# Optimization experiments

Hardware: AMD Instinct MI355X
Metric: run time of the kernel (lower is better)

Reference implementation:

```python
import jax, jax.numpy as jnp
import numpy as np

N_NODES = 50000
N_EDGES = 800000
N_GRAPHS = 256
D_IN, D_H1, D_H2, D_OUT = 64, 64, 64, 64


def gcn_conv(x, W, b, src, dst, n_nodes):
    # PyG GCNConv (eval): h = x @ W; add self-loops; deg[i] = in_deg(i) + 1;
    # out[i] = sum_{j->i} h[j] * deg[i]^-1/2 deg[j]^-1/2 + h[i]/deg[i] + b
    h = x @ W  # [N, F]
    ones = jnp.ones((src.shape[0],), dtype=x.dtype)
    deg = jax.ops.segment_sum(ones, dst, num_segments=n_nodes) + 1.0  # self loop
    dinv = jax.lax.rsqrt(deg)
    norm = dinv[src] * dinv[dst]  # [E]
    msg = h[src] * norm[:, None]  # [E, F]  (memory-bound gather)
    agg = jax.ops.segment_sum(msg, dst, num_segments=n_nodes)  # scatter-add
    agg = agg + h * (1.0 / deg)[:, None]  # self-loop contribution
    return agg + b


def setup_inputs() -> dict:
    key = jax.random.key(0)
    ks = jax.random.split(key, 12)
    x = jax.random.normal(ks[0], (N_NODES, D_IN), dtype=jnp.float32)
    src = jax.random.randint(ks[1], (N_EDGES,), 0, N_NODES)
    dst = jax.random.randint(ks[2], (N_EDGES,), 0, N_NODES)
    batch = jnp.sort(jax.random.randint(ks[3], (N_NODES,), 0, N_GRAPHS))
    def glorot(k, fin, fout):
        s = jnp.sqrt(6.0 / (fin + fout))
        return jax.random.uniform(k, (fin, fout), jnp.float32, -s, s)
    return {
        "x": x, "src": src, "dst": dst, "batch": batch,
        "W1": glorot(ks[4], D_IN, D_H1), "b1": jnp.zeros((D_H1,), jnp.float32),
        "W2": glorot(ks[5], D_H1, D_H2), "b2": jnp.zeros((D_H2,), jnp.float32),
        "W3": glorot(ks[6], D_H2, D_OUT), "b3": jnp.zeros((D_OUT,), jnp.float32),
        "Wl": glorot(ks[7], D_OUT, 1), "bl": jnp.zeros((1,), jnp.float32),
    }


def reference(x, src, dst, batch, W1, b1, W2, b2, W3, b3, Wl, bl):
    n = x.shape[0]
    h = jax.nn.relu(gcn_conv(x, W1, b1, src, dst, n))   # dropout inactive (eval)
    h = jax.nn.relu(gcn_conv(h, W2, b2, src, dst, n))
    h = jax.nn.relu(gcn_conv(h, W3, b3, src, dst, n))
    # global_mean_pool over graph ids
    sums = jax.ops.segment_sum(h, batch, num_segments=N_GRAPHS)  # [G, F]
    cnt = jax.ops.segment_sum(jnp.ones((n,), h.dtype), batch, num_segments=N_GRAPHS)
    pooled = sums / jnp.maximum(cnt, 1.0)[:, None]
    return pooled @ Wl + bl  # [G, 1]
```

## Files before the change

kernel.cpp:

```cpp
#include <hip/hip_runtime.h>

#define N_NODES 50000
#define N_EDGES 800000
#define N_GRAPHS 256
#define F 64
#define NBUCK 196
#define CAP 4608
#define P3_TILE 2048
#define P3_GRID ((N_EDGES + P3_TILE - 1) / P3_TILE)
#define BCAP 6144

__device__ __forceinline__ unsigned short f2bf(float f) {
    union { float f; unsigned u; } c; c.f = f;
    unsigned u = c.u + 0x7FFFu + ((c.u >> 16) & 1u);
    return (unsigned short)(u >> 16);
}
__device__ __forceinline__ unsigned pack2bf(float lo, float hi) {
    return (unsigned)f2bf(lo) | ((unsigned)f2bf(hi) << 16);
}
__device__ __forceinline__ float bfl(unsigned u) {
    union { unsigned u; float f; } c; c.u = u << 16; return c.f;
}
__device__ __forceinline__ float bfh(unsigned u) {
    union { unsigned u; float f; } c; c.u = u & 0xFFFF0000u; return c.f;
}

__global__ __launch_bounds__(256) void partition_edges(const int* __restrict__ src,
                                                       const int* __restrict__ dst,
                                                       int* __restrict__ bcur,
                                                       unsigned int* __restrict__ bpair) {
    __shared__ int bh[NBUCK], bloc[NBUCK], bpos[NBUCK];
    int t = threadIdx.x;
    int lo = blockIdx.x * P3_TILE;
    int hi = min(lo + P3_TILE, N_EDGES);
    for (int i = t; i < NBUCK; i += 256) { bh[i] = 0; bpos[i] = 0; }
    __syncthreads();
    for (int e = lo + t; e < hi; e += 256) atomicAdd(&bh[dst[e] >> 8], 1);
    __syncthreads();
    for (int i = t; i < NBUCK; i += 256)
        bloc[i] = bh[i] ? atomicAdd(&bcur[i], bh[i]) : 0;
    __syncthreads();
    for (int e = lo + t; e < hi; e += 256) {
        int d = dst[e];
        int b = d >> 8;
        int r = atomicAdd(&bpos[b], 1);
        bpair[(size_t)b * CAP + bloc[b] + r] = ((unsigned)src[e] << 8) | (unsigned)(d & 255);
    }
}

__global__ __launch_bounds__(256) void bucket_sort(const unsigned int* __restrict__ bpair,
                                                   const int* __restrict__ bcur,
                                                   int* __restrict__ eidx,
                                                   int* __restrict__ rbeg,
                                                   int* __restrict__ rend,
                                                   float* __restrict__ dinv) {
    __shared__ int cnt[256], s[256], pos[256];
    __shared__ int lout[BCAP];
    int b = blockIdx.x, t = threadIdx.x;
    int base = b * CAP;
    int sz = bcur[b];

    cnt[t] = 0;
    __syncthreads();
    for (int i = t; i < sz; i += 256) atomicAdd(&cnt[bpair[base + i] & 255], 1);
    __syncthreads();
    int v = cnt[t];
    s[t] = v;
    __syncthreads();
    for (int off = 1; off < 256; off <<= 1) {
        int u = (t >= off) ? s[t - off] : 0;
        __syncthreads();
        s[t] += u;
        __syncthreads();
    }
    int excl = s[t] - v;
    pos[t] = excl;
    int node = b * 256 + t;
    if (node < N_NODES) {
        rbeg[node] = base + excl;
        rend[node] = base + excl + v;
        dinv[node] = 1.0f / sqrtf((float)v + 1.0f);
    }
    __syncthreads();

    if (sz <= BCAP) {
        for (int i = t; i < sz; i += 256) {
            unsigned p = bpair[base + i];
            int r = atomicAdd(&pos[p & 255], 1);
            lout[r] = (int)((p >> 8) << 7);
        }
        __syncthreads();
        for (int i = t; i < sz; i += 256) eidx[base + i] = lout[i];
    } else {
        for (int i = t; i < sz; i += 256) {
            unsigned p = bpair[base + i];
            int r = atomicAdd(&pos[p & 255], 1);
            eidx[base + r] = (int)((p >> 8) << 7);
        }
    }
}

#define XSTRIDE 17
template <bool BF16IN>
__global__ __launch_bounds__(256) void gemm64_t(const void* __restrict__ Xv,
                                                const float* __restrict__ W,
                                                const float* __restrict__ dinv,
                                                unsigned short* __restrict__ Hn, int n) {
    __shared__ float4 sW[64 * 16];
    __shared__ float4 sX[128 * XSTRIDE];
    int tid = threadIdx.x;
    int base = blockIdx.x * 128;

    const float4* W4 = (const float4*)W;
    for (int i = tid; i < 64 * 16; i += 256) sW[i] = W4[i];
    if (BF16IN) {
        const uint4* X4 = (const uint4*)Xv;
        for (int i = tid; i < 128 * 8; i += 256) {
            int r = i >> 3, c = i & 7;
            int node = base + r;
            uint4 u = (node < n) ? X4[(size_t)node * 8 + c]
                                 : make_uint4(0u, 0u, 0u, 0u);
            sX[r * XSTRIDE + 2 * c]     = make_float4(bfl(u.x), bfh(u.x), bfl(u.y), bfh(u.y));
            sX[r * XSTRIDE + 2 * c + 1] = make_float4(bfl(u.z), bfh(u.z), bfl(u.w), bfh(u.w));
        }
    } else {
        const float4* X4 = (const float4*)Xv;
        for (int i = tid; i < 128 * 16; i += 256) {
            int r = i >> 4, kg = i & 15;
            int node = base + r;
            sX[r * XSTRIDE + kg] = (node < n) ? X4[(size_t)node * 16 + kg]
                                              : make_float4(0.f, 0.f, 0.f, 0.f);
        }
    }
    __syncthreads();

    int fg = tid & 15;
    int ng = tid >> 4;
    float4 acc[8];
#pragma unroll
    for (int ii = 0; ii < 8; ii++) acc[ii] = make_float4(0.f, 0.f, 0.f, 0.f);

    for (int kg = 0; kg < 16; kg++) {
        float4 xv[8];
#pragma unroll
        for (int ii = 0; ii < 8; ii++) xv[ii] = sX[(ng + 16 * ii) * XSTRIDE + kg];
#pragma unroll
        for (int kk = 0; kk < 4; kk++) {
            float4 wv = sW[(4 * kg + kk) * 16 + fg];
#pragma unroll
            for (int ii = 0; ii < 8; ii++) {
                float xs = (kk == 0) ? xv[ii].x : (kk == 1) ? xv[ii].y
                         : (kk == 2) ? xv[ii].z : xv[ii].w;
                acc[ii].x += wv.x * xs;
                acc[ii].y += wv.y * xs;
                acc[ii].z += wv.z * xs;
                acc[ii].w += wv.w * xs;
            }
        }
    }

    ushort4* H4 = (ushort4*)Hn;
#pragma unroll
    for (int ii = 0; ii < 8; ii++) {
        int node = base + ng + 16 * ii;
        if (node < n) {
            float d = dinv[node];
            float4 o = acc[ii];
            ushort4 u;
            u.x = f2bf(o.x * d); u.y = f2bf(o.y * d);
            u.z = f2bf(o.z * d); u.w = f2bf(o.w * d);
            H4[(size_t)node * 16 + fg] = u;
        }
    }
}

__global__ __launch_bounds__(256) void gather_layer(const int* __restrict__ rbeg,
                                                    const int* __restrict__ rend,
                                                    const int* __restrict__ eidx,
                                                    const float* __restrict__ dinv,
                                                    const unsigned short* __restrict__ Hn,
                                                    const float* __restrict__ b,
                                                    unsigned short* __restrict__ OUT, int n) {
    int wv = (blockIdx.x * blockDim.x + threadIdx.x) >> 6;
    int lane = threadIdx.x & 63;
    int ns = lane >> 3, f = lane & 7;
    int node = wv * 8 + ns;
    bool valid = node < n;
    int beg = valid ? rbeg[node] : 0;
    int end = valid ? rend[node] : 0;
    const char* Hb = (const char*)Hn;

    float a0 = 0.f, a1 = 0.f, a2 = 0.f, a3 = 0.f;
    float a4 = 0.f, a5 = 0.f, a6 = 0.f, a7 = 0.f;
    int k = beg;
    for (; k + 3 < end; k += 4) {
        int o1 = eidx[k], o2 = eidx[k + 1], o3 = eidx[k + 2], o4 = eidx[k + 3];
        uint4 p = *(const uint4*)(Hb + o1 + f * 16);
        uint4 q = *(const uint4*)(Hb + o2 + f * 16);
        uint4 r = *(const uint4*)(Hb + o3 + f * 16);
        uint4 w = *(const uint4*)(Hb + o4 + f * 16);
        a0 += (bfl(p.x) + bfl(q.x)) + (bfl(r.x) + bfl(w.x));
        a1 += (bfh(p.x) + bfh(q.x)) + (bfh(r.x) + bfh(w.x));
        a2 += (bfl(p.y) + bfl(q.y)) + (bfl(r.y) + bfl(w.y));
        a3 += (bfh(p.y) + bfh(q.y)) + (bfh(r.y) + bfh(w.y));
        a4 += (bfl(p.z) + bfl(q.z)) + (bfl(r.z) + bfl(w.z));
        a5 += (bfh(p.z) + bfh(q.z)) + (bfh(r.z) + bfh(w.z));
        a6 += (bfl(p.w) + bfl(q.w)) + (bfl(r.w) + bfl(w.w));
        a7 += (bfh(p.w) + bfh(q.w)) + (bfh(r.w) + bfh(w.w));
    }
    for (; k < end; k++) {
        int o1 = eidx[k];
        uint4 p = *(const uint4*)(Hb + o1 + f * 16);
        a0 += bfl(p.x); a1 += bfh(p.x);
        a2 += bfl(p.y); a3 += bfh(p.y);
        a4 += bfl(p.z); a5 += bfh(p.z);
        a6 += bfl(p.w); a7 += bfh(p.w);
    }

    if (valid) {
        float di = dinv[node];
        uint4 hs = *(const uint4*)(Hb + (size_t)node * 128 + f * 16);
        float4 b0 = ((const float4*)b)[2 * f];
        float4 b1 = ((const float4*)b)[2 * f + 1];
        float v0 = fmaxf(di * (a0 + bfl(hs.x)) + b0.x, 0.f);
        float v1 = fmaxf(di * (a1 + bfh(hs.x)) + b0.y, 0.f);
        float v2 = fmaxf(di * (a2 + bfl(hs.y)) + b0.z, 0.f);
        float v3 = fmaxf(di * (a3 + bfh(hs.y)) + b0.w, 0.f);
        float v4 = fmaxf(di * (a4 + bfl(hs.z)) + b1.x, 0.f);
        float v5 = fmaxf(di * (a5 + bfh(hs.z)) + b1.y, 0.f);
        float v6 = fmaxf(di * (a6 + bfl(hs.w)) + b1.z, 0.f);
        float v7 = fmaxf(di * (a7 + bfh(hs.w)) + b1.w, 0.f);
        uint4 u;
        u.x = pack2bf(v0, v1); u.y = pack2bf(v2, v3);
        u.z = pack2bf(v4, v5); u.w = pack2bf(v6, v7);
        ((uint4*)OUT)[(size_t)node * 8 + f] = u;
    }
}

__global__ __launch_bounds__(256) void gather_pool(const int* __restrict__ rbeg,
                                                   const int* __restrict__ rend,
                                                   const int* __restrict__ eidx,
                                                   const float* __restrict__ dinv,
                                                   const unsigned short* __restrict__ Hn,
                                                   const float* __restrict__ b,
                                                   const float* __restrict__ Wl,
                                                   float* __restrict__ pdot, int n) {
    int wv = (blockIdx.x * blockDim.x + threadIdx.x) >> 6;
    int lane = threadIdx.x & 63;
    int ns = lane >> 3, f = lane & 7;
    int node = wv * 8 + ns;
    bool valid = node < n;
    int beg = valid ? rbeg[node] : 0;
    int end = valid ? rend[node] : 0;
    const char* Hb = (const char*)Hn;

    float a0 = 0.f, a1 = 0.f, a2 = 0.f, a3 = 0.f;
    float a4 = 0.f, a5 = 0.f, a6 = 0.f, a7 = 0.f;
    int k = beg;
    for (; k + 3 < end; k += 4) {
        int o1 = eidx[k], o2 = eidx[k + 1], o3 = eidx[k + 2], o4 = eidx[k + 3];
        uint4 p = *(const uint4*)(Hb + o1 + f * 16);
        uint4 q = *(const uint4*)(Hb + o2 + f * 16);
        uint4 r = *(const uint4*)(Hb + o3 + f * 16);
        uint4 w = *(const uint4*)(Hb + o4 + f * 16);
        a0 += (bfl(p.x) + bfl(q.x)) + (bfl(r.x) + bfl(w.x));
        a1 += (bfh(p.x) + bfh(q.x)) + (bfh(r.x) + bfh(w.x));
        a2 += (bfl(p.y) + bfl(q.y)) + (bfl(r.y) + bfl(w.y));
        a3 += (bfh(p.y) + bfh(q.y)) + (bfh(r.y) + bfh(w.y));
        a4 += (bfl(p.z) + bfl(q.z)) + (bfl(r.z) + bfl(w.z));
        a5 += (bfh(p.z) + bfh(q.z)) + (bfh(r.z) + bfh(w.z));
        a6 += (bfl(p.w) + bfl(q.w)) + (bfl(r.w) + bfl(w.w));
        a7 += (bfh(p.w) + bfh(q.w)) + (bfh(r.w) + bfh(w.w));
    }
    for (; k < end; k++) {
        int o1 = eidx[k];
        uint4 p = *(const uint4*)(Hb + o1 + f * 16);
        a0 += bfl(p.x); a1 += bfh(p.x);
        a2 += bfl(p.y); a3 += bfh(p.y);
        a4 += bfl(p.z); a5 += bfh(p.z);
        a6 += bfl(p.w); a7 += bfh(p.w);
    }

    float di = valid ? dinv[node] : 0.f;
    uint4 hs = valid ? *(const uint4*)(Hb + (size_t)node * 128 + f * 16)
                     : make_uint4(0u, 0u, 0u, 0u);
    float4 b0 = ((const float4*)b)[2 * f];
    float4 b1 = ((const float4*)b)[2 * f + 1];
    float4 w0 = ((const float4*)Wl)[2 * f];
    float4 w1 = ((const float4*)Wl)[2 * f + 1];
    float d = 0.f;
    d += fmaxf(di * (a0 + bfl(hs.x)) + b0.x, 0.f) * w0.x;
    d += fmaxf(di * (a1 + bfh(hs.x)) + b0.y, 0.f) * w0.y;
    d += fmaxf(di * (a2 + bfl(hs.y)) + b0.z, 0.f) * w0.z;
    d += fmaxf(di * (a3 + bfh(hs.y)) + b0.w, 0.f) * w0.w;
    d += fmaxf(di * (a4 + bfl(hs.z)) + b1.x, 0.f) * w1.x;
    d += fmaxf(di * (a5 + bfh(hs.z)) + b1.y, 0.f) * w1.y;
    d += fmaxf(di * (a6 + bfl(hs.w)) + b1.z, 0.f) * w1.z;
    d += fmaxf(di * (a7 + bfh(hs.w)) + b1.w, 0.f) * w1.w;
#pragma unroll
    for (int m = 1; m <= 4; m <<= 1) d += __shfl_xor(d, m);
    if (valid && f == 0) pdot[node] = d;
}

__global__ __launch_bounds__(64) void final_out(const float* __restrict__ pdot,
                                                const int* __restrict__ batch,
                                                const float* __restrict__ bl,
                                                float* __restrict__ out) {
    int g = blockIdx.x;
    __shared__ int slo, shi;
    int lane = threadIdx.x;
    if (lane == 0) {
        int a = 0, b = N_NODES;
        while (a < b) { int m = (a + b) >> 1; if (batch[m] < g) a = m + 1; else b = m; }
        slo = a;
        b = N_NODES;
        while (a < b) { int m = (a + b) >> 1; if (batch[m] < g + 1) a = m + 1; else b = m; }
        shi = a;
    }
    __syncthreads();
    int lo = slo, hi = shi;
    float acc = 0.f;
    for (int i = lo + lane; i < hi; i += 64) acc += pdot[i];
#pragma unroll
    for (int off = 32; off > 0; off >>= 1) acc += __shfl_down(acc, off);
    if (lane == 0) {
        float cnt = (float)(hi - lo);
        out[g] = acc / fmaxf(cnt, 1.0f) + bl[0];
    }
}

extern "C" void kernel_launch(void* const* d_in, const int* in_sizes, int n_in,
                              void* d_out, int out_size, void* d_ws, size_t ws_size,
                              hipStream_t stream) {
    const float* x     = (const float*)d_in[0];
    const int*   src   = (const int*)d_in[1];
    const int*   dst   = (const int*)d_in[2];
    const int*   batch = (const int*)d_in[3];
    const float* W1 = (const float*)d_in[4];  const float* b1 = (const float*)d_in[5];
    const float* W2 = (const float*)d_in[6];  const float* b2 = (const float*)d_in[7];
    const float* W3 = (const float*)d_in[8];  const float* b3 = (const float*)d_in[9];
    const float* Wl = (const float*)d_in[10]; const float* bl = (const float*)d_in[11];
    float* out = (float*)d_out;

    char* ws = (char*)d_ws;
    unsigned short* Abf = (unsigned short*)ws;
    unsigned short* Bbf = Abf + (size_t)N_NODES * F;
    float* dinv    = (float*)(Bbf + (size_t)N_NODES * F);
    float* pdot    = dinv + N_NODES;
    int*   rbeg    = (int*)(pdot + N_NODES);
    int*   rend    = rbeg + N_NODES;
    int*   bcur    = rend + N_NODES;
    unsigned int* bpair = (unsigned int*)(bcur + NBUCK);
    int*   eidx    = (int*)(bpair + (size_t)NBUCK * CAP);

    const int GEMM_GRID   = (N_NODES + 127) / 128;
    const int GATHER_GRID = (N_NODES + 31) / 32;

    hipMemsetAsync(bcur, 0, NBUCK * sizeof(int), stream);
    partition_edges<<<P3_GRID, 256, 0, stream>>>(src, dst, bcur, bpair);
    bucket_sort<<<NBUCK, 256, 0, stream>>>(bpair, bcur, eidx, rbeg, rend, dinv);

    gemm64_t<false><<<GEMM_GRID, 256, 0, stream>>>((const void*)x, W1, dinv, Abf, N_NODES);
    gather_layer<<<GATHER_GRID, 256, 0, stream>>>(rbeg, rend, eidx, dinv, Abf, b1, Bbf, N_NODES);

    gemm64_t<true><<<GEMM_GRID, 256, 0, stream>>>((const void*)Bbf, W2, dinv, Abf, N_NODES);
    gather_layer<<<GATHER_GRID, 256, 0, stream>>>(rbeg, rend, eidx, dinv, Abf, b2, Bbf, N_NODES);

    gemm64_t<true><<<GEMM_GRID, 256, 0, stream>>>((const void*)Bbf, W3, dinv, Abf, N_NODES);
    gather_pool<<<GATHER_GRID, 256, 0, stream>>>(rbeg, rend, eidx, dinv, Abf, b3, Wl, pdot, N_NODES);

    final_out<<<N_GRAPHS, 64, 0, stream>>>(pdot, batch, bl, out);
}
```

Before: 210.7 us.

## Pad CSR rows to multiples of four with a zero sentinel node for vectorized gathers

Each node's edge list is padded to a multiple of four entries, and the padding points to an extra all-zero row appended after the feature buffer. The gather kernels can then drop their scalar tail loop and load four indices with a single int4 read. The cost is extra wasted gathers of the zero row, a larger per-bucket capacity, and a bucket sort that now always stages through shared memory. That last step assumes the padded bucket size fits within BCAP.

```diff
diff --git a/kernel.cpp b/kernel.cpp
--- a/kernel.cpp
+++ b/kernel.cpp
@@ -5,10 +5,11 @@
 #define N_GRAPHS 256
 #define F 64
 #define NBUCK 196
-#define CAP 4608
+#define CAP 5120
 #define P3_TILE 2048
 #define P3_GRID ((N_EDGES + P3_TILE - 1) / P3_TILE)
 #define BCAP 6144
+#define ZOFF (N_NODES * 128)
 
 __device__ __forceinline__ unsigned short f2bf(float f) {
     union { float f; unsigned u; } c; c.f = f;
@@ -53,19 +54,23 @@
                                                    int* __restrict__ eidx,
                                                    int* __restrict__ rbeg,
                                                    int* __restrict__ rend,
-                                                   float* __restrict__ dinv) {
+                                                   float* __restrict__ dinv,
+                                                   unsigned short* __restrict__ Abf) {
     __shared__ int cnt[256], s[256], pos[256];
     __shared__ int lout[BCAP];
     int b = blockIdx.x, t = threadIdx.x;
     int base = b * CAP;
     int sz = bcur[b];
 
+    if (b == 0 && t < 8) ((uint4*)Abf)[(size_t)N_NODES * 8 + t] = make_uint4(0u, 0u, 0u, 0u);
+
     cnt[t] = 0;
     __syncthreads();
     for (int i = t; i < sz; i += 256) atomicAdd(&cnt[bpair[base + i] & 255], 1);
     __syncthreads();
     int v = cnt[t];
-    s[t] = v;
+    int pv = (v + 3) & ~3;
+    s[t] = pv;
     __syncthreads();
     for (int off = 1; off < 256; off <<= 1) {
         int u = (t >= off) ? s[t - off] : 0;
@@ -73,31 +78,26 @@
         s[t] += u;
         __syncthreads();
     }
-    int excl = s[t] - v;
+    int excl = s[t] - pv;
     pos[t] = excl;
     int node = b * 256 + t;
     if (node < N_NODES) {
         rbeg[node] = base + excl;
-        rend[node] = base + excl + v;
+        rend[node] = base + excl + pv;
         dinv[node] = 1.0f / sqrtf((float)v + 1.0f);
     }
-    __syncthreads();
-
-    if (sz <= BCAP) {
-        for (int i = t; i < sz; i += 256) {
-            unsigned p = bpair[base + i];
-            int r = atomicAdd(&pos[p & 255], 1);
-            lout[r] = (int)((p >> 8) << 7);
-        }
-        __syncthreads();
-        for (int i = t; i < sz; i += 256) eidx[base + i] = lout[i];
-    } else {
-        for (int i = t; i < sz; i += 256) {
-            unsigned p = bpair[base + i];
-            int r = atomicAdd(&pos[p & 255], 1);
-            eidx[base + r] = (int)((p >> 8) << 7);
-        }
-    }
+    int padtot = s[255];
+    __syncthreads();
+
+    for (int i = t; i < sz; i += 256) {
+        unsigned p = bpair[base + i];
+        int r = atomicAdd(&pos[p & 255], 1);
+        lout[r] = (int)((p >> 8) << 7);
+    }
+    __syncthreads();
+    for (int j = v; j < pv; j++) lout[excl + j] = ZOFF;
+    __syncthreads();
+    for (int i = t; i < padtot; i += 256) eidx[base + i] = lout[i];
 }
 
 #define XSTRIDE 17
@@ -192,13 +192,12 @@
 
     float a0 = 0.f, a1 = 0.f, a2 = 0.f, a3 = 0.f;
     float a4 = 0.f, a5 = 0.f, a6 = 0.f, a7 = 0.f;
-    int k = beg;
-    for (; k + 3 < end; k += 4) {
-        int o1 = eidx[k], o2 = eidx[k + 1], o3 = eidx[k + 2], o4 = eidx[k + 3];
-        uint4 p = *(const uint4*)(Hb + o1 + f * 16);
-        uint4 q = *(const uint4*)(Hb + o2 + f * 16);
-        uint4 r = *(const uint4*)(Hb + o3 + f * 16);
-        uint4 w = *(const uint4*)(Hb + o4 + f * 16);
+    for (int k = beg; k < end; k += 4) {
+        int4 o = *(const int4*)(eidx + k);
+        uint4 p = *(const uint4*)(Hb + o.x + f * 16);
+        uint4 q = *(const uint4*)(Hb + o.y + f * 16);
+        uint4 r = *(const uint4*)(Hb + o.z + f * 16);
+        uint4 w = *(const uint4*)(Hb + o.w + f * 16);
         a0 += (bfl(p.x) + bfl(q.x)) + (bfl(r.x) + bfl(w.x));
         a1 += (bfh(p.x) + bfh(q.x)) + (bfh(r.x) + bfh(w.x));
         a2 += (bfl(p.y) + bfl(q.y)) + (bfl(r.y) + bfl(w.y));
@@ -207,14 +206,6 @@
         a5 += (bfh(p.z) + bfh(q.z)) + (bfh(r.z) + bfh(w.z));
         a6 += (bfl(p.w) + bfl(q.w)) + (bfl(r.w) + bfl(w.w));
         a7 += (bfh(p.w) + bfh(q.w)) + (bfh(r.w) + bfh(w.w));
-    }
-    for (; k < end; k++) {
-        int o1 = eidx[k];
-        uint4 p = *(const uint4*)(Hb + o1 + f * 16);
-        a0 += bfl(p.x); a1 += bfh(p.x);
-        a2 += bfl(p.y); a3 += bfh(p.y);
-        a4 += bfl(p.z); a5 += bfh(p.z);
-        a6 += bfl(p.w); a7 += bfh(p.w);
     }
 
     if (valid) {
@@ -256,13 +247,12 @@
 
     float a0 = 0.f, a1 = 0.f, a2 = 0.f, a3 = 0.f;
     float a4 = 0.f, a5 = 0.f, a6 = 0.f, a7 = 0.f;
-    int k = beg;
-    for (; k + 3 < end; k += 4) {
-        int o1 = eidx[k], o2 = eidx[k + 1], o3 = eidx[k + 2], o4 = eidx[k + 3];
-        uint4 p = *(const uint4*)(Hb + o1 + f * 16);
-        uint4 q = *(const uint4*)(Hb + o2 + f * 16);
-        uint4 r = *(const uint4*)(Hb + o3 + f * 16);
-        uint4 w = *(const uint4*)(Hb + o4 + f * 16);
+    for (int k = beg; k < end; k += 4) {
+        int4 o = *(const int4*)(eidx + k);
+        uint4 p = *(const uint4*)(Hb + o.x + f * 16);
+        uint4 q = *(const uint4*)(Hb + o.y + f * 16);
+        uint4 r = *(const uint4*)(Hb + o.z + f * 16);
+        uint4 w = *(const uint4*)(Hb + o.w + f * 16);
         a0 += (bfl(p.x) + bfl(q.x)) + (bfl(r.x) + bfl(w.x));
         a1 += (bfh(p.x) + bfh(q.x)) + (bfh(r.x) + bfh(w.x));
         a2 += (bfl(p.y) + bfl(q.y)) + (bfl(r.y) + bfl(w.y));
@@ -271,14 +261,6 @@
         a5 += (bfh(p.z) + bfh(q.z)) + (bfh(r.z) + bfh(w.z));
         a6 += (bfl(p.w) + bfl(q.w)) + (bfl(r.w) + bfl(w.w));
         a7 += (bfh(p.w) + bfh(q.w)) + (bfh(r.w) + bfh(w.w));
-    }
-    for (; k < end; k++) {
-        int o1 = eidx[k];
-        uint4 p = *(const uint4*)(Hb + o1 + f * 16);
-        a0 += bfl(p.x); a1 += bfh(p.x);
-        a2 += bfl(p.y); a3 += bfh(p.y);
-        a4 += bfl(p.z); a5 += bfh(p.z);
-        a6 += bfl(p.w); a7 += bfh(p.w);
     }
 
     float di = valid ? dinv[node] : 0.f;
@@ -344,7 +326,7 @@
 
     char* ws = (char*)d_ws;
     unsigned short* Abf = (unsigned short*)ws;
-    unsigned short* Bbf = Abf + (size_t)N_NODES * F;
+    unsigned short* Bbf = Abf + (size_t)(N_NODES + 1) * F;
     float* dinv    = (float*)(Bbf + (size_t)N_NODES * F);
     float* pdot    = dinv + N_NODES;
     int*   rbeg    = (int*)(pdot + N_NODES);
@@ -358,7 +340,7 @@
 
     hipMemsetAsync(bcur, 0, NBUCK * sizeof(int), stream);
     partition_edges<<<P3_GRID, 256, 0, stream>>>(src, dst, bcur, bpair);
-    bucket_sort<<<NBUCK, 256, 0, stream>>>(bpair, bcur, eidx, rbeg, rend, dinv);
+    bucket_sort<<<NBUCK, 256, 0, stream>>>(bpair, bcur, eidx, rbeg, rend, dinv, Abf);
 
     gemm64_t<false><<<GEMM_GRID, 256, 0, stream>>>((const void*)x, W1, dinv, Abf, N_NODES);
     gather_layer<<<GATHER_GRID, 256, 0, stream>>>(rbeg, rend, eidx, dinv, Abf, b1, Bbf, N_NODES);
```

New measurement: 209.2 us (median of 2 runs). No clear change (-0.7%).
